# Performance work log

Measured on AMD Instinct MI355X. Metric: run time of the kernel, lower is better.

Reference implementation:

```python
import jax, jax.numpy as jnp
import numpy as np

BXYZ = 4
L = 1_000_000
C = 64
KERNEL = 2
N_BATCH = 4
GRID = 1024


def setup_inputs() -> dict:
    key = jax.random.key(0)
    k1, k2, k3 = jax.random.split(key, 3)
    in_feats = jax.random.normal(k1, (L, C), dtype=jnp.float32)
    b = jax.random.randint(k2, (L, 1), 0, N_BATCH, dtype=jnp.int32)
    xyz = jax.random.randint(k3, (L, 3), 0, GRID, dtype=jnp.int32)
    in_coords = jnp.concatenate([b, xyz], axis=1)  # [L, 4] = (batch, x, y, z)
    return {"in_feats": in_feats, "in_coords": in_coords, "kernel_size": KERNEL}


def _encode(coords):
    # mixed-radix encoding: (((b)*X + x)*Y + y)*Z + z with per-dim extents
    min_c = coords.min(axis=0)            # [4]
    c = coords - min_c
    max_c = c.max(axis=0) + 1             # [4] radices
    enc = c[:, 0]
    for i in range(1, BXYZ):
        enc = enc * max_c[i] + c[:, i]
    return enc, min_c, max_c


def _decode(enc, min_c, max_c):
    cols = []
    for idx in range(BXYZ - 1, -1, -1):
        rem = enc % max_c[idx]
        cols.append(min_c[idx] + rem)
        enc = (enc - rem) // max_c[idx]
    return jnp.stack(cols[::-1], axis=1)  # [L*, 4]


def reference(in_feats, in_coords, kernel_size):
    # downsample spatial coords (keep batch column)
    coords = in_coords.at[:, 1:].set(in_coords[:, 1:] // kernel_size)
    enc, min_c, max_c = _encode(coords)
    n = enc.shape[0]
    # jit-compatible unique padded to n (torch returns only the unique rows;
    # here trailing padded rows carry -inf feats / fill coords)
    uniq, inv = jnp.unique(enc, return_inverse=True, size=n, fill_value=0)
    out_feats = jnp.full((n, in_feats.shape[1]), -jnp.inf, dtype=in_feats.dtype)
    out_feats = out_feats.at[inv].max(in_feats)  # scatter-amax, include_self=False
    out_coords = _decode(uniq, min_c, max_c)
    return out_feats, out_coords
```

## Files before the change

### kernel.cpp

```cpp
#include <hip/hip_runtime.h>
#include <climits>
#include <cstdint>
#include <cstddef>
#include <math.h>


static constexpr int kNumGroups = 1 << 21;
static constexpr int kNumWords  = 1 << 24;
static constexpr size_t kBitmapBytes = (size_t)kNumWords * 4;

typedef float f32x4 __attribute__((ext_vector_type(4)));

#define GS(i, n) for (int i = blockIdx.x * blockDim.x + threadIdx.x; i < (n); i += gridDim.x * blockDim.x)

__global__ void k_init(int* wsi) {
    int t = threadIdx.x;
    if (t < 4) wsi[t] = INT_MAX;
    else if (t < 8) wsi[t] = INT_MIN;
}

__global__ void k_minmax(const int4* __restrict__ coords, const int* __restrict__ ksp,
                         int L, int* wsi) {
    int ks = *ksp;
    int mn[4] = {INT_MAX, INT_MAX, INT_MAX, INT_MAX};
    int mx[4] = {INT_MIN, INT_MIN, INT_MIN, INT_MIN};
    GS(i, L) {
        int4 c = coords[i];
        int v0 = c.x, v1 = c.y / ks, v2 = c.z / ks, v3 = c.w / ks;
        mn[0] = min(mn[0], v0); mx[0] = max(mx[0], v0);
        mn[1] = min(mn[1], v1); mx[1] = max(mx[1], v1);
        mn[2] = min(mn[2], v2); mx[2] = max(mx[2], v2);
        mn[3] = min(mn[3], v3); mx[3] = max(mx[3], v3);
    }
    #pragma unroll
    for (int off = 32; off; off >>= 1) {
        #pragma unroll
        for (int k = 0; k < 4; ++k) {
            mn[k] = min(mn[k], __shfl_down(mn[k], off));
            mx[k] = max(mx[k], __shfl_down(mx[k], off));
        }
    }
    __shared__ int smn[16], smx[16];
    int wave = threadIdx.x >> 6, lane = threadIdx.x & 63;
    if (lane == 0) {
        #pragma unroll
        for (int k = 0; k < 4; ++k) { smn[wave * 4 + k] = mn[k]; smx[wave * 4 + k] = mx[k]; }
    }
    __syncthreads();
    if (threadIdx.x < 4) {
        int k = threadIdx.x;
        int a = min(min(smn[k], smn[4 + k]), min(smn[8 + k], smn[12 + k]));
        int b = max(max(smx[k], smx[4 + k]), max(smx[8 + k], smx[12 + k]));
        atomicMin(&wsi[k], a);
        atomicMax(&wsi[4 + k], b);
    }
}

__global__ void k_scalars(int* wsi) {
    if (threadIdx.x == 0 && blockIdx.x == 0) {
        int m1 = wsi[5] - wsi[1] + 1;
        int m2 = wsi[6] - wsi[2] + 1;
        int m3 = wsi[7] - wsi[3] + 1;
        wsi[8] = m1; wsi[9] = m2; wsi[10] = m3;
    }
}

__global__ void k_encode(const int4* __restrict__ coords, const int* __restrict__ ksp, int L,
                         const int* __restrict__ wsi, unsigned* __restrict__ enc,
                         unsigned* __restrict__ bitmap) {
    int ks = *ksp;
    int mn0 = wsi[0], mn1 = wsi[1], mn2 = wsi[2], mn3 = wsi[3];
    unsigned m1 = (unsigned)wsi[8], m2 = (unsigned)wsi[9], m3 = (unsigned)wsi[10];
    GS(i, L) {
        int4 c = coords[i];
        unsigned c0 = (unsigned)(c.x - mn0);
        unsigned c1 = (unsigned)(c.y / ks - mn1);
        unsigned c2 = (unsigned)(c.z / ks - mn2);
        unsigned c3 = (unsigned)(c.w / ks - mn3);
        unsigned e = ((c0 * m1 + c1) * m2 + c2) * m3 + c3;
        unsigned bit = 1u << (e & 31u);
        unsigned old = atomicOr(&bitmap[e >> 5], bit);
        enc[i] = e | ((old & bit) ? 0x80000000u : 0u);
    }
}

__global__ void k_groupcnt(const unsigned* __restrict__ bitmap,
                           unsigned* __restrict__ gcnt, unsigned* __restrict__ ctaSums) {
    int g = blockIdx.x * blockDim.x + threadIdx.x;
    const uint4* p = (const uint4*)(bitmap + ((size_t)g << 3));
    uint4 a = p[0], b = p[1];
    unsigned s = __popc(a.x) + __popc(a.y) + __popc(a.z) + __popc(a.w)
               + __popc(b.x) + __popc(b.y) + __popc(b.z) + __popc(b.w);
    gcnt[g] = s;
    __shared__ unsigned sm[256];
    sm[threadIdx.x] = s;
    __syncthreads();
    for (int off = 128; off; off >>= 1) {
        if (threadIdx.x < off) sm[threadIdx.x] += sm[threadIdx.x + off];
        __syncthreads();
    }
    if (threadIdx.x == 0) ctaSums[blockIdx.x] = sm[0];
}

__global__ void k_scan_cta(const unsigned* __restrict__ ctaSums, unsigned* __restrict__ ctaPref,
                           int* wsi) {
    int t = threadIdx.x;
    unsigned v[8]; unsigned ts = 0;
    #pragma unroll
    for (int j = 0; j < 8; ++j) { v[j] = ctaSums[t * 8 + j]; ts += v[j]; }
    __shared__ unsigned sm[1024];
    sm[t] = ts;
    __syncthreads();
    for (int off = 1; off < 1024; off <<= 1) {
        unsigned add = (t >= off) ? sm[t - off] : 0u;
        __syncthreads();
        sm[t] += add;
        __syncthreads();
    }
    unsigned run = sm[t] - ts;
    #pragma unroll
    for (int j = 0; j < 8; ++j) { ctaPref[t * 8 + j] = run; run += v[j]; }
    if (t == 1023) wsi[14] = (int)sm[1023];
}

__global__ void k_gpref(const unsigned* __restrict__ gcnt, const unsigned* __restrict__ ctaPref,
                        unsigned* __restrict__ gpref) {
    int g = blockIdx.x * blockDim.x + threadIdx.x;
    int t = threadIdx.x;
    unsigned v = gcnt[g];
    __shared__ unsigned sm[256];
    sm[t] = v;
    __syncthreads();
    for (int off = 1; off < 256; off <<= 1) {
        unsigned add = (t >= off) ? sm[t - off] : 0u;
        __syncthreads();
        sm[t] += add;
        __syncthreads();
    }
    gpref[g] = ctaPref[blockIdx.x] + sm[t] - v;
}

__global__ void k_rank(const unsigned* __restrict__ enc, const unsigned* __restrict__ bitmap,
                       const unsigned* __restrict__ gpref, int L,
                       unsigned* __restrict__ inv, unsigned* __restrict__ srcrow) {
    GS(i, L) {
        unsigned ei = enc[i];
        unsigned dup = ei & 0x80000000u;
        unsigned e = ei & 0x1FFFFFFFu;
        unsigned w = e >> 5, g = w >> 3, wb = w & 7u;
        const uint4* p = (const uint4*)(bitmap + ((size_t)g << 3));
        uint4 a = p[0], b = p[1];
        unsigned r = gpref[g];
        r += (wb > 0) ? __popc(a.x) : 0u;
        r += (wb > 1) ? __popc(a.y) : 0u;
        r += (wb > 2) ? __popc(a.z) : 0u;
        r += (wb > 3) ? __popc(a.w) : 0u;
        r += (wb > 4) ? __popc(b.x) : 0u;
        r += (wb > 5) ? __popc(b.y) : 0u;
        r += (wb > 6) ? __popc(b.z) : 0u;
        unsigned word = bitmap[w];
        r += __popc(word & ((1u << (e & 31u)) - 1u));
        inv[i] = r | dup;
        if (!dup) srcrow[r] = (unsigned)i;
    }
}

__global__ void k_coords(const unsigned* __restrict__ bitmap, const unsigned* __restrict__ gpref,
                         const int* __restrict__ wsi, float* __restrict__ outc) {
    int g = blockIdx.x * blockDim.x + threadIdx.x;
    const uint4* p = (const uint4*)(bitmap + ((size_t)g << 3));
    uint4 a = p[0], b4 = p[1];
    unsigned wv[8] = {a.x, a.y, a.z, a.w, b4.x, b4.y, b4.z, b4.w};
    unsigned rank = gpref[g];
    unsigned m1 = (unsigned)wsi[8], m2 = (unsigned)wsi[9], m3 = (unsigned)wsi[10];
    int mn0 = wsi[0], mn1 = wsi[1], mn2 = wsi[2], mn3 = wsi[3];
    #pragma unroll
    for (int j = 0; j < 8; ++j) {
        unsigned bits = wv[j];
        unsigned wbase = (((unsigned)g << 3) + (unsigned)j) << 5;
        while (bits) {
            unsigned b = (unsigned)__ffs(bits) - 1u;
            bits &= bits - 1u;
            unsigned code = wbase | b;
            unsigned c3 = code % m3; code /= m3;
            unsigned c2 = code % m2; code /= m2;
            unsigned c1 = code % m1; code /= m1;
            float4 o = make_float4((float)(mn0 + (int)code), (float)(mn1 + (int)c1),
                                   (float)(mn2 + (int)c2), (float)(mn3 + (int)c3));
            ((float4*)outc)[rank] = o;
            rank++;
        }
    }
}

__global__ void k_pad(const int* __restrict__ wsi, int L, float* __restrict__ outc) {
    int K = wsi[14];
    float4 o = make_float4((float)wsi[0], (float)wsi[1], (float)wsi[2], (float)wsi[3]);
    GS(r, L) {
        if (r >= K) ((float4*)outc)[r] = o;
    }
}

__global__ void k_gather3(const f32x4* __restrict__ feats4, const unsigned* __restrict__ srcrow,
                          const int* __restrict__ wsi, int L, f32x4* __restrict__ out4) {
    int wpb = blockDim.x >> 6;
    int gw = gridDim.x * wpb;
    int w = blockIdx.x * wpb + (threadIdx.x >> 6);
    int lane = threadIdx.x & 63;
    int sub = lane >> 4;
    int q   = lane & 15;
    int K = wsi[14];
    const int RPI = 16;
    for (int r0 = w * RPI; r0 < L; r0 += gw * RPI) {
        int r[4]; unsigned s[4];
        #pragma unroll
        for (int j = 0; j < 4; ++j) {
            r[j] = r0 + j * 4 + sub;
            s[j] = (r[j] < K) ? srcrow[r[j]] : 0xFFFFFFFFu;
        }
        f32x4 v[4];
        #pragma unroll
        for (int j = 0; j < 4; ++j) {
            v[j] = (s[j] != 0xFFFFFFFFu) ? feats4[(size_t)s[j] * 16 + q]
                                         : (f32x4){0.f, 0.f, 0.f, 0.f};
        }
        #pragma unroll
        for (int j = 0; j < 4; ++j)
            if (r[j] < L) __builtin_nontemporal_store(v[j], &out4[(size_t)r[j] * 16 + q]);
    }
}

__global__ void k_gather3_gen(const float* __restrict__ feats, const unsigned* __restrict__ srcrow,
                              const int* __restrict__ wsi, int L, int C, float* __restrict__ out) {
    int wpb = blockDim.x >> 6;
    int gw = gridDim.x * wpb;
    int w = blockIdx.x * wpb + (threadIdx.x >> 6);
    int lane = threadIdx.x & 63;
    int K = wsi[14];
    for (int r = w; r < L; r += gw) {
        if (r < K) {
            unsigned s = srcrow[r];
            for (int cc = lane; cc < C; cc += 64)
                out[(size_t)r * C + cc] = feats[(size_t)s * C + cc];
        } else {
            for (int cc = lane; cc < C; cc += 64) out[(size_t)r * C + cc] = 0.0f;
        }
    }
}

__device__ inline void atomicMaxFloat(float* addr, float val) {
    unsigned* ua = (unsigned*)addr;
    unsigned old = *((volatile unsigned*)ua);
    while (__uint_as_float(old) < val) {
        unsigned assumed = old;
        old = atomicCAS(ua, assumed, __float_as_uint(val));
        if (old == assumed) break;
    }
}

__global__ void k_fix(const float* __restrict__ feats, const unsigned* __restrict__ inv,
                      int L, int C, float* __restrict__ out) {
    int lane = threadIdx.x & 63;
    int stride = gridDim.x * blockDim.x;
    for (int i = blockIdx.x * blockDim.x + threadIdx.x; i - lane < L; i += stride) {
        unsigned e = (i < L) ? inv[i] : 0u;
        bool multi = (e >> 31) != 0u;
        unsigned long long mask = __ballot(multi);
        while (mask) {
            int srcl = __ffsll((unsigned long long)mask) - 1;
            mask &= mask - 1ull;
            int id = __shfl(i, srcl);
            int row = __shfl((int)(e & 0x7FFFFFFFu), srcl);
            for (int cc = lane; cc < C; cc += 64)
                atomicMaxFloat(&out[(size_t)row * C + cc], feats[(size_t)id * C + cc]);
        }
    }
}

extern "C" void kernel_launch(void* const* d_in, const int* in_sizes, int n_in,
                              void* d_out, int out_size, void* d_ws, size_t ws_size,
                              hipStream_t stream) {
    const float* feats = (const float*)d_in[0];
    const int4* coords = (const int4*)d_in[1];
    const int* ksp     = (const int*)d_in[2];
    int L = in_sizes[1] / 4;
    int C = in_sizes[0] / L;

    char* ob = (char*)d_out;
    unsigned* bitmap = (unsigned*)ob;
    unsigned* gcnt   = (unsigned*)(ob + kBitmapBytes);
    unsigned* gpref  = gcnt + kNumGroups;
    unsigned* enc    = gpref + kNumGroups;
    float* out_feats  = (float*)d_out;
    float* out_coords = out_feats + (size_t)L * C;

    char* wsb = (char*)d_ws;
    int* wsi = (int*)wsb;
    unsigned* ctaSums = (unsigned*)(wsb + 4096);
    unsigned* ctaPref = (unsigned*)(wsb + 4096 + 32768);
    unsigned* inv     = (unsigned*)(wsb + (1 << 20));
    unsigned* srcrow  = inv + L;

    (void)hipMemsetAsync(bitmap, 0, kBitmapBytes, stream);
    k_init<<<1, 64, 0, stream>>>(wsi);
    k_minmax<<<256, 256, 0, stream>>>(coords, ksp, L, wsi);
    k_scalars<<<1, 1, 0, stream>>>(wsi);
    k_encode<<<1024, 256, 0, stream>>>(coords, ksp, L, wsi, enc, bitmap);
    k_groupcnt<<<kNumGroups / 256, 256, 0, stream>>>(bitmap, gcnt, ctaSums);
    k_scan_cta<<<1, 1024, 0, stream>>>(ctaSums, ctaPref, wsi);
    k_gpref<<<kNumGroups / 256, 256, 0, stream>>>(gcnt, ctaPref, gpref);
    k_rank<<<1024, 256, 0, stream>>>(enc, bitmap, gpref, L, inv, srcrow);
    k_coords<<<kNumGroups / 256, 256, 0, stream>>>(bitmap, gpref, wsi, out_coords);
    k_pad<<<1024, 256, 0, stream>>>(wsi, L, out_coords);
    if (C == 64)
        k_gather3<<<2048, 256, 0, stream>>>((const f32x4*)feats, srcrow, wsi, L, (f32x4*)out_feats);
    else
        k_gather3_gen<<<2048, 256, 0, stream>>>(feats, srcrow, wsi, L, C, out_feats);
    k_fix<<<2048, 256, 0, stream>>>(feats, inv, L, C, out_feats);
}
```

Before: 285.6 us.

## Fuse prefix, coords and pad kernels; drop scalars kernel; vectorize rank; deepen gather unroll

Removes the k_scalars launch by computing radices inline. It drops the gcnt array and recomputes popcounts in a fused kernel that also writes group prefixes, decodes coordinates and pads the tail rows, which replaces three launches with one. k_rank now handles four entries per thread with a vector load of enc and reuses the already-loaded bitmap words instead of reloading one. The gather unroll doubles to 8 rows per wave with nontemporal feature loads, which increases memory-level parallelism at the cost of more registers.

```diff
diff --git a/kernel.cpp b/kernel.cpp
--- a/kernel.cpp
+++ b/kernel.cpp
@@ -56,21 +56,14 @@
     }
 }
 
-__global__ void k_scalars(int* wsi) {
-    if (threadIdx.x == 0 && blockIdx.x == 0) {
-        int m1 = wsi[5] - wsi[1] + 1;
-        int m2 = wsi[6] - wsi[2] + 1;
-        int m3 = wsi[7] - wsi[3] + 1;
-        wsi[8] = m1; wsi[9] = m2; wsi[10] = m3;
-    }
-}
-
 __global__ void k_encode(const int4* __restrict__ coords, const int* __restrict__ ksp, int L,
                          const int* __restrict__ wsi, unsigned* __restrict__ enc,
                          unsigned* __restrict__ bitmap) {
     int ks = *ksp;
     int mn0 = wsi[0], mn1 = wsi[1], mn2 = wsi[2], mn3 = wsi[3];
-    unsigned m1 = (unsigned)wsi[8], m2 = (unsigned)wsi[9], m3 = (unsigned)wsi[10];
+    unsigned m1 = (unsigned)(wsi[5] - mn1 + 1);
+    unsigned m2 = (unsigned)(wsi[6] - mn2 + 1);
+    unsigned m3 = (unsigned)(wsi[7] - mn3 + 1);
     GS(i, L) {
         int4 c = coords[i];
         unsigned c0 = (unsigned)(c.x - mn0);
@@ -84,14 +77,12 @@
     }
 }
 
-__global__ void k_groupcnt(const unsigned* __restrict__ bitmap,
-                           unsigned* __restrict__ gcnt, unsigned* __restrict__ ctaSums) {
+__global__ void k_groupcnt(const unsigned* __restrict__ bitmap, unsigned* __restrict__ ctaSums) {
     int g = blockIdx.x * blockDim.x + threadIdx.x;
     const uint4* p = (const uint4*)(bitmap + ((size_t)g << 3));
     uint4 a = p[0], b = p[1];
     unsigned s = __popc(a.x) + __popc(a.y) + __popc(a.z) + __popc(a.w)
                + __popc(b.x) + __popc(b.y) + __popc(b.z) + __popc(b.w);
-    gcnt[g] = s;
     __shared__ unsigned sm[256];
     sm[threadIdx.x] = s;
     __syncthreads();
@@ -123,13 +114,19 @@
     if (t == 1023) wsi[14] = (int)sm[1023];
 }
 
-__global__ void k_gpref(const unsigned* __restrict__ gcnt, const unsigned* __restrict__ ctaPref,
-                        unsigned* __restrict__ gpref) {
+__global__ void k_gpref_coords(const unsigned* __restrict__ bitmap,
+                               const unsigned* __restrict__ ctaPref,
+                               const int* __restrict__ wsi,
+                               unsigned* __restrict__ gpref,
+                               float* __restrict__ outc, int L) {
     int g = blockIdx.x * blockDim.x + threadIdx.x;
+    const uint4* p = (const uint4*)(bitmap + ((size_t)g << 3));
+    uint4 a = p[0], b4 = p[1];
+    unsigned s = __popc(a.x) + __popc(a.y) + __popc(a.z) + __popc(a.w)
+               + __popc(b4.x) + __popc(b4.y) + __popc(b4.z) + __popc(b4.w);
+    __shared__ unsigned sm[256];
     int t = threadIdx.x;
-    unsigned v = gcnt[g];
-    __shared__ unsigned sm[256];
-    sm[t] = v;
+    sm[t] = s;
     __syncthreads();
     for (int off = 1; off < 256; off <<= 1) {
         unsigned add = (t >= off) ? sm[t - off] : 0u;
@@ -137,43 +134,14 @@
         sm[t] += add;
         __syncthreads();
     }
-    gpref[g] = ctaPref[blockIdx.x] + sm[t] - v;
-}
-
-__global__ void k_rank(const unsigned* __restrict__ enc, const unsigned* __restrict__ bitmap,
-                       const unsigned* __restrict__ gpref, int L,
-                       unsigned* __restrict__ inv, unsigned* __restrict__ srcrow) {
-    GS(i, L) {
-        unsigned ei = enc[i];
-        unsigned dup = ei & 0x80000000u;
-        unsigned e = ei & 0x1FFFFFFFu;
-        unsigned w = e >> 5, g = w >> 3, wb = w & 7u;
-        const uint4* p = (const uint4*)(bitmap + ((size_t)g << 3));
-        uint4 a = p[0], b = p[1];
-        unsigned r = gpref[g];
-        r += (wb > 0) ? __popc(a.x) : 0u;
-        r += (wb > 1) ? __popc(a.y) : 0u;
-        r += (wb > 2) ? __popc(a.z) : 0u;
-        r += (wb > 3) ? __popc(a.w) : 0u;
-        r += (wb > 4) ? __popc(b.x) : 0u;
-        r += (wb > 5) ? __popc(b.y) : 0u;
-        r += (wb > 6) ? __popc(b.z) : 0u;
-        unsigned word = bitmap[w];
-        r += __popc(word & ((1u << (e & 31u)) - 1u));
-        inv[i] = r | dup;
-        if (!dup) srcrow[r] = (unsigned)i;
-    }
-}
-
-__global__ void k_coords(const unsigned* __restrict__ bitmap, const unsigned* __restrict__ gpref,
-                         const int* __restrict__ wsi, float* __restrict__ outc) {
-    int g = blockIdx.x * blockDim.x + threadIdx.x;
-    const uint4* p = (const uint4*)(bitmap + ((size_t)g << 3));
-    uint4 a = p[0], b4 = p[1];
+    unsigned rank = ctaPref[blockIdx.x] + sm[t] - s;
+    gpref[g] = rank;
+
+    int mn0 = wsi[0], mn1 = wsi[1], mn2 = wsi[2], mn3 = wsi[3];
+    unsigned m1 = (unsigned)(wsi[5] - mn1 + 1);
+    unsigned m2 = (unsigned)(wsi[6] - mn2 + 1);
+    unsigned m3 = (unsigned)(wsi[7] - mn3 + 1);
     unsigned wv[8] = {a.x, a.y, a.z, a.w, b4.x, b4.y, b4.z, b4.w};
-    unsigned rank = gpref[g];
-    unsigned m1 = (unsigned)wsi[8], m2 = (unsigned)wsi[9], m3 = (unsigned)wsi[10];
-    int mn0 = wsi[0], mn1 = wsi[1], mn2 = wsi[2], mn3 = wsi[3];
     #pragma unroll
     for (int j = 0; j < 8; ++j) {
         unsigned bits = wv[j];
@@ -191,13 +159,44 @@
             rank++;
         }
     }
-}
-
-__global__ void k_pad(const int* __restrict__ wsi, int L, float* __restrict__ outc) {
     int K = wsi[14];
-    float4 o = make_float4((float)wsi[0], (float)wsi[1], (float)wsi[2], (float)wsi[3]);
-    GS(r, L) {
-        if (r >= K) ((float4*)outc)[r] = o;
+    float4 o = make_float4((float)mn0, (float)mn1, (float)mn2, (float)mn3);
+    int total = gridDim.x * blockDim.x;
+    for (int r = K + g; r < L; r += total)
+        ((float4*)outc)[r] = o;
+}
+
+__global__ void k_rank(const unsigned* __restrict__ enc, const unsigned* __restrict__ bitmap,
+                       const unsigned* __restrict__ gpref, int L,
+                       unsigned* __restrict__ inv, unsigned* __restrict__ srcrow) {
+    int t = blockIdx.x * blockDim.x + threadIdx.x;
+    int base = t * 4;
+    if (base >= L) return;
+    uint4 ev = *(const uint4*)(enc + base);
+    unsigned es[4] = {ev.x, ev.y, ev.z, ev.w};
+    #pragma unroll
+    for (int j = 0; j < 4; ++j) {
+        int i = base + j;
+        if (i >= L) break;
+        unsigned ei = es[j];
+        unsigned dup = ei & 0x80000000u;
+        unsigned e = ei & 0x1FFFFFFFu;
+        unsigned w = e >> 5, g = w >> 3, wb = w & 7u;
+        const uint4* p = (const uint4*)(bitmap + ((size_t)g << 3));
+        uint4 a = p[0], b = p[1];
+        unsigned r = gpref[g];
+        r += (wb > 0) ? __popc(a.x) : 0u;
+        r += (wb > 1) ? __popc(a.y) : 0u;
+        r += (wb > 2) ? __popc(a.z) : 0u;
+        r += (wb > 3) ? __popc(a.w) : 0u;
+        r += (wb > 4) ? __popc(b.x) : 0u;
+        r += (wb > 5) ? __popc(b.y) : 0u;
+        r += (wb > 6) ? __popc(b.z) : 0u;
+        unsigned word = (wb < 4) ? ((wb < 2) ? (wb == 0 ? a.x : a.y) : (wb == 2 ? a.z : a.w))
+                                 : ((wb < 6) ? (wb == 4 ? b.x : b.y) : (wb == 6 ? b.z : b.w));
+        r += __popc(word & ((1u << (e & 31u)) - 1u));
+        inv[i] = r | dup;
+        if (!dup) srcrow[r] = (unsigned)i;
     }
 }
 
@@ -210,22 +209,24 @@
     int sub = lane >> 4;
     int q   = lane & 15;
     int K = wsi[14];
-    const int RPI = 16;
+    const int U = 8;
+    const int RPI = 4 * U;
     for (int r0 = w * RPI; r0 < L; r0 += gw * RPI) {
-        int r[4]; unsigned s[4];
-        #pragma unroll
-        for (int j = 0; j < 4; ++j) {
+        int r[U]; unsigned s[U];
+        #pragma unroll
+        for (int j = 0; j < U; ++j) {
             r[j] = r0 + j * 4 + sub;
             s[j] = (r[j] < K) ? srcrow[r[j]] : 0xFFFFFFFFu;
         }
-        f32x4 v[4];
-        #pragma unroll
-        for (int j = 0; j < 4; ++j) {
-            v[j] = (s[j] != 0xFFFFFFFFu) ? feats4[(size_t)s[j] * 16 + q]
-                                         : (f32x4){0.f, 0.f, 0.f, 0.f};
-        }
-        #pragma unroll
-        for (int j = 0; j < 4; ++j)
+        f32x4 v[U];
+        #pragma unroll
+        for (int j = 0; j < U; ++j) {
+            v[j] = (s[j] != 0xFFFFFFFFu)
+                     ? __builtin_nontemporal_load(&feats4[(size_t)s[j] * 16 + q])
+                     : (f32x4){0.f, 0.f, 0.f, 0.f};
+        }
+        #pragma unroll
+        for (int j = 0; j < U; ++j)
             if (r[j] < L) __builtin_nontemporal_store(v[j], &out4[(size_t)r[j] * 16 + q]);
     }
 }
@@ -288,8 +289,7 @@
 
     char* ob = (char*)d_out;
     unsigned* bitmap = (unsigned*)ob;
-    unsigned* gcnt   = (unsigned*)(ob + kBitmapBytes);
-    unsigned* gpref  = gcnt + kNumGroups;
+    unsigned* gpref  = (unsigned*)(ob + kBitmapBytes);
     unsigned* enc    = gpref + kNumGroups;
     float* out_feats  = (float*)d_out;
     float* out_coords = out_feats + (size_t)L * C;
@@ -304,14 +304,11 @@
     (void)hipMemsetAsync(bitmap, 0, kBitmapBytes, stream);
     k_init<<<1, 64, 0, stream>>>(wsi);
     k_minmax<<<256, 256, 0, stream>>>(coords, ksp, L, wsi);
-    k_scalars<<<1, 1, 0, stream>>>(wsi);
     k_encode<<<1024, 256, 0, stream>>>(coords, ksp, L, wsi, enc, bitmap);
-    k_groupcnt<<<kNumGroups / 256, 256, 0, stream>>>(bitmap, gcnt, ctaSums);
+    k_groupcnt<<<kNumGroups / 256, 256, 0, stream>>>(bitmap, ctaSums);
     k_scan_cta<<<1, 1024, 0, stream>>>(ctaSums, ctaPref, wsi);
-    k_gpref<<<kNumGroups / 256, 256, 0, stream>>>(gcnt, ctaPref, gpref);
-    k_rank<<<1024, 256, 0, stream>>>(enc, bitmap, gpref, L, inv, srcrow);
-    k_coords<<<kNumGroups / 256, 256, 0, stream>>>(bitmap, gpref, wsi, out_coords);
-    k_pad<<<1024, 256, 0, stream>>>(wsi, L, out_coords);
+    k_gpref_coords<<<kNumGroups / 256, 256, 0, stream>>>(bitmap, ctaPref, wsi, gpref, out_coords, L);
+    k_rank<<<(L + 1023) / 1024, 256, 0, stream>>>(enc, bitmap, gpref, L, inv, srcrow);
     if (C == 64)
         k_gather3<<<2048, 256, 0, stream>>>((const f32x4*)feats, srcrow, wsi, L, (f32x4*)out_feats);
     else
```

Result: faster. 274.0 us (-4.1%).
